# Kernel tuning notes

Hardware: AMD Instinct MI355X
Metric: run time of the kernel (lower is better)

## Reference

```python
import jax, jax.numpy as jnp
import numpy as np

B = 65536          # number of 17-node circle graphs in the batch
NN = 17            # nodes per graph (hardcoded in module)
FEAT = 32          # feature_num


def _circle_edge_index(num_graphs):
    s = np.arange(NN)
    d = (s + 1) % NN
    src0 = np.concatenate([s, d])   # bidirectional ring
    dst0 = np.concatenate([d, s])
    off = (np.arange(num_graphs) * NN)[:, None]
    src = (src0[None, :] + off).ravel()
    dst = (dst0[None, :] + off).ravel()
    return jnp.asarray(np.stack([src, dst]).astype(np.int32))


def setup_inputs() -> dict:
    key = jax.random.key(0)
    ks = jax.random.split(key, 10)
    p = lambda k, shp, fan: jax.random.normal(k, shp, jnp.float32) / np.sqrt(fan)
    return {
        "z": jax.random.normal(ks[0], (B, FEAT), jnp.float32),
        "edge_index": _circle_edge_index(B),                      # [2, 2*17*B]
        "fc_w": p(ks[1], (FEAT, NN * 8), FEAT),
        "fc_b": jnp.zeros((NN * 8,), jnp.float32),
        "w1": p(ks[2], (8, 16), 8),
        "b1": jnp.zeros((16,), jnp.float32),
        "w2": p(ks[3], (16, 32), 16),
        "b2": jnp.zeros((32,), jnp.float32),
        "w3": p(ks[4], (32, FEAT), 32),
        "b3": jnp.zeros((FEAT,), jnp.float32),
    }


def _gcn(x, src, tgt, norm, W, b, n_nodes):
    # GCNConv: out[t] = sum_{(s,t)} norm(s,t) * (x[s] @ W) + b
    h = x @ W
    msg = h[src] * norm[:, None]
    return jax.ops.segment_sum(msg, tgt, num_segments=n_nodes) + b


def reference(z, edge_index, fc_w, fc_b, w1, b1, w2, b2, w3, b3):
    n_nodes = z.shape[0] * NN
    # fc_expand then reshape to node features [N, 8]
    x = (z @ fc_w + fc_b).reshape(-1, 8)
    # symmetric GCN normalization with added self-loops (same for all 3 convs)
    loop = jnp.arange(n_nodes, dtype=edge_index.dtype)
    src = jnp.concatenate([edge_index[0], loop])
    tgt = jnp.concatenate([edge_index[1], loop])
    deg = jax.ops.segment_sum(jnp.ones_like(tgt, dtype=x.dtype), tgt,
                              num_segments=n_nodes)
    dinv = jax.lax.rsqrt(deg)  # deg >= 1 because of self-loops
    norm = dinv[src] * dinv[tgt]
    x = jax.nn.relu(_gcn(x, src, tgt, norm, w1, b1, n_nodes))
    x = jax.nn.relu(_gcn(x, src, tgt, norm, w2, b2, n_nodes))
    x = _gcn(x, src, tgt, norm, w3, b3, n_nodes)
    return x.reshape(-1, NN, FEAT)
```

## Files before the change

### kernel.cpp

```cpp
#include <hip/hip_runtime.h>
#include <stdint.h>

typedef unsigned short u16;
typedef unsigned int   u32;
typedef __attribute__((ext_vector_type(8))) short bf16x8;
typedef __attribute__((ext_vector_type(4))) float f32x4;

#define NN   17
#define G    16
#define ROWS (G*NN)
#define TPB  256
#define XS   40

__device__ u16   g_fcw_frag[9*512];
__device__ float g_fcb_agg[144];
__device__ u16   g_w1_frag[512];
__device__ u16   g_w2_frag[2*512];
__device__ u16   g_w3_frag[2*512];
__device__ float g_bias1[16];
__device__ float g_bias2[32];
__device__ float g_bias3[32];

__device__ __forceinline__ float uf(u32 u){ union{u32 a; float b;} c; c.a=u; return c.b; }
__device__ __forceinline__ u32   fu(float f){ union{float a; u32 b;} c; c.a=f; return c.b; }
__device__ __forceinline__ u16 f2bf(float f){
    u32 u = fu(f);
    return (u16)((u + 0x7FFFu + ((u >> 16) & 1u)) >> 16);
}
__device__ __forceinline__ bf16x8 as_bf16x8(uint4 v){ union{uint4 a; bf16x8 b;} c; c.a=v; return c.b; }

__device__ __forceinline__ u32 ringsum3(u32 a, u32 b, u32 c){
    const u32 M = 0xFFFF0000u;
    float hs = uf(a & M) + uf(b & M) + uf(c & M);
    float ls = uf(a << 16) + uf(b << 16) + uf(c << 16);
    u32 uh = fu(hs); uh = (uh + 0x7FFFu + ((uh >> 16) & 1u)) & M;
    u32 ul = fu(ls); ul = (ul + 0x7FFFu + ((ul >> 16) & 1u)) >> 16;
    return uh | ul;
}

__global__ void gnn_prep(const float* __restrict__ fcw, const float* __restrict__ fcb,
                         const float* __restrict__ w1,  const float* __restrict__ b1,
                         const float* __restrict__ w2,  const float* __restrict__ b2,
                         const float* __restrict__ w3,  const float* __restrict__ b3)
{
    const int t = threadIdx.x;
    const float inv3 = 1.0f/3.0f;
    for (int e = t; e < 9*512; e += TPB) {
        int tile = e >> 9, ln = (e >> 3) & 63, j = e & 7;
        int n = tile*16 + (ln & 15), k = (ln >> 4)*8 + j;
        u16 v = 0;
        if (n < 136) {
            int i = n >> 3, f = n & 7;
            int im = (i == 0    ? NN-1 : i-1)*8 + f;
            int ip = (i == NN-1 ? 0    : i+1)*8 + f;
            v = f2bf((fcw[k*136 + im] + fcw[k*136 + n] + fcw[k*136 + ip]) * inv3);
        }
        g_fcw_frag[e] = v;
    }
    if (t < 144) {
        float v = 0.f;
        if (t < 136) {
            int i = t >> 3, f = t & 7;
            int im = (i == 0    ? NN-1 : i-1)*8 + f;
            int ip = (i == NN-1 ? 0    : i+1)*8 + f;
            v = (fcb[im] + fcb[t] + fcb[ip]) * inv3;
        }
        g_fcb_agg[t] = v;
    }
    for (int e = t; e < 512; e += TPB) {
        int ln = e >> 3, j = e & 7;
        int k = (ln >> 4)*8 + j, n = ln & 15;
        g_w1_frag[e] = (k < 8) ? f2bf(w1[k*16 + n]) : (u16)0;
    }
    for (int e = t; e < 1024; e += TPB) {
        int h = e >> 9, ln = (e >> 3) & 63, j = e & 7;
        int k = ((ln >> 4))*8 + j, c = 2*(ln & 15) + h;
        g_w2_frag[e] = (k < 16) ? f2bf(w2[k*32 + c] * inv3) : (u16)0;
        g_w3_frag[e] = f2bf(w3[k*32 + c] * inv3);
    }
    if (t < 16)                 g_bias1[t]    = b1[t];
    else if (t >= 32 && t < 64) g_bias2[t-32] = b2[t-32];
    else if (t >= 64 && t < 96) g_bias3[t-64] = b3[t-64];
}

__global__ __launch_bounds__(TPB, 3)
void gnn_main(const float* __restrict__ z, float* __restrict__ out, int nG)
{
    __shared__ u16 xb0[ROWS*XS];
    __shared__ u16 xb1[ROWS*XS];
    __shared__ u16 zt [G*XS];

    const int t = threadIdx.x, wv = t >> 6, ln = t & 63;
    const int quad = ln >> 4, l16 = ln & 15;
    int gmax = nG - blockIdx.x * G; if (gmax > G) gmax = G;

    bf16x8 fw1  = *(const bf16x8*)(g_w1_frag + ln*8);
    bf16x8 fw2e = *(const bf16x8*)(g_w2_frag + ln*8);
    bf16x8 fw2o = *(const bf16x8*)(g_w2_frag + 512 + ln*8);
    bf16x8 fw3e = *(const bf16x8*)(g_w3_frag + ln*8);
    bf16x8 fw3o = *(const bf16x8*)(g_w3_frag + 512 + ln*8);
    bf16x8 ffc[3]; float fcbv[3];
    #pragma unroll
    for (int s = 0; s < 3; ++s) {
        int tile = wv + 4*s;
        if (tile < 9) {
            ffc[s]  = *(const bf16x8*)(g_fcw_frag + tile*512 + ln*8);
            fcbv[s] = g_fcb_agg[tile*16 + l16];
        } else { ffc[s] = (bf16x8){0,0,0,0,0,0,0,0}; fcbv[s] = 0.f; }
    }
    const float bias1 = g_bias1[l16];
    const float b2e = g_bias2[2*l16], b2o = g_bias2[2*l16+1];
    const float b3e = g_bias3[2*l16], b3o = g_bias3[2*l16+1];

    const float* zg = z + (size_t)blockIdx.x * (G*32);
    for (int el = t; el < G*32; el += TPB)
        if (el < gmax*32) zt[(el >> 5)*XS + (el & 31)] = f2bf(zg[el]);
    __syncthreads();

    {
        bf16x8 az = *(const bf16x8*)&zt[l16*XS + quad*8];
        #pragma unroll
        for (int s = 0; s < 3; ++s) {
            int tile = wv + 4*s;
            if (tile < 9) {
                f32x4 cb = {fcbv[s], fcbv[s], fcbv[s], fcbv[s]};
                f32x4 d = __builtin_amdgcn_mfma_f32_16x16x32_bf16(az, ffc[s], cb, 0, 0, 0);
                int n = tile*16 + l16;
                if (n < 136) {
                    int node = n >> 3, f = n & 7;
                    #pragma unroll
                    for (int r = 0; r < 4; ++r) {
                        int gg = quad*4 + r;
                        xb0[(gg*NN + node)*XS + f] = f2bf(d[r]);
                    }
                }
            }
        }
    }
    __syncthreads();

    {
        f32x4 cb = {bias1, bias1, bias1, bias1};
        #pragma unroll
        for (int s = 0; s < 5; ++s) {
            int tile = wv + 4*s;
            if (tile < 17) {
                bf16x8 af = {0,0,0,0,0,0,0,0};
                if (quad == 0) af = *(const bf16x8*)&xb0[(tile*16 + l16)*XS];
                f32x4 d = __builtin_amdgcn_mfma_f32_16x16x32_bf16(af, fw1, cb, 0, 0, 0);
                #pragma unroll
                for (int r = 0; r < 4; ++r) {
                    int rr = tile*16 + quad*4 + r;
                    xb1[rr*XS + l16] = f2bf(fmaxf(d[r], 0.f));
                }
            }
        }
    }
    __syncthreads();

    {
        f32x4 cbe = {b2e,b2e,b2e,b2e}, cbo = {b2o,b2o,b2o,b2o};
        #pragma unroll
        for (int s = 0; s < 5; ++s) {
            int tile = wv + 4*s;
            if (tile < 17) {
                bf16x8 af = {0,0,0,0,0,0,0,0};
                if (quad < 2) {
                    int rr = tile*16 + l16;
                    int gg = (rr*3856) >> 16; int i = rr - gg*NN;
                    int rm = rr + (i == 0    ? NN-1 : -1);
                    int rp = rr + (i == NN-1 ? 1-NN  :  1);
                    uint4 A  = *(const uint4*)&xb1[rm*XS + quad*8];
                    uint4 Bv = *(const uint4*)&xb1[rr*XS + quad*8];
                    uint4 Cv = *(const uint4*)&xb1[rp*XS + quad*8];
                    af = as_bf16x8(make_uint4(ringsum3(A.x,Bv.x,Cv.x), ringsum3(A.y,Bv.y,Cv.y),
                                              ringsum3(A.z,Bv.z,Cv.z), ringsum3(A.w,Bv.w,Cv.w)));
                }
                f32x4 d0 = __builtin_amdgcn_mfma_f32_16x16x32_bf16(af, fw2e, cbe, 0, 0, 0);
                f32x4 d1 = __builtin_amdgcn_mfma_f32_16x16x32_bf16(af, fw2o, cbo, 0, 0, 0);
                u32* ob = (u32*)xb0;
                #pragma unroll
                for (int r = 0; r < 4; ++r) {
                    int rr2 = tile*16 + quad*4 + r;
                    u32 ue = fu(fmaxf(d0[r], 0.f));
                    u32 uo = fu(fmaxf(d1[r], 0.f));
                    ue = (ue + 0x7FFFu + ((ue >> 16) & 1u)) >> 16;
                    uo = (uo + 0x7FFFu + ((uo >> 16) & 1u)) & 0xFFFF0000u;
                    ob[rr2*(XS/2) + l16] = ue | uo;
                }
            }
        }
    }
    __syncthreads();

    {
        f32x4 cbe = {b3e,b3e,b3e,b3e}, cbo = {b3o,b3o,b3o,b3o};
        float* ob = out + (size_t)blockIdx.x * (ROWS*32);
        const int rowmax = gmax * NN;
        #pragma unroll
        for (int s = 0; s < 5; ++s) {
            int tile = wv + 4*s;
            if (tile < 17) {
                int rr = tile*16 + l16;
                int gg = (rr*3856) >> 16; int i = rr - gg*NN;
                int rm = rr + (i == 0    ? NN-1 : -1);
                int rp = rr + (i == NN-1 ? 1-NN  :  1);
                uint4 A  = *(const uint4*)&xb0[rm*XS + quad*8];
                uint4 Bv = *(const uint4*)&xb0[rr*XS + quad*8];
                uint4 Cv = *(const uint4*)&xb0[rp*XS + quad*8];
                bf16x8 af = as_bf16x8(make_uint4(ringsum3(A.x,Bv.x,Cv.x), ringsum3(A.y,Bv.y,Cv.y),
                                                 ringsum3(A.z,Bv.z,Cv.z), ringsum3(A.w,Bv.w,Cv.w)));
                f32x4 d0 = __builtin_amdgcn_mfma_f32_16x16x32_bf16(af, fw3e, cbe, 0, 0, 0);
                f32x4 d1 = __builtin_amdgcn_mfma_f32_16x16x32_bf16(af, fw3o, cbo, 0, 0, 0);
                #pragma unroll
                for (int r = 0; r < 4; ++r) {
                    int rr2 = tile*16 + quad*4 + r;
                    if (rr2 < rowmax) {
                        float2 v = make_float2(d0[r], d1[r]);
                        *(float2*)&ob[(size_t)rr2*32 + 2*l16] = v;
                    }
                }
            }
        }
    }
}

extern "C" void kernel_launch(void* const* d_in, const int* in_sizes, int n_in,
                              void* d_out, int out_size, void* d_ws, size_t ws_size,
                              hipStream_t stream) {
    const float* z    = (const float*)d_in[0];
    const float* fcw  = (const float*)d_in[2];
    const float* fcb  = (const float*)d_in[3];
    const float* w1   = (const float*)d_in[4];
    const float* b1   = (const float*)d_in[5];
    const float* w2   = (const float*)d_in[6];
    const float* b2   = (const float*)d_in[7];
    const float* w3   = (const float*)d_in[8];
    const float* b3   = (const float*)d_in[9];
    float* out = (float*)d_out;

    const int nG   = in_sizes[0] / 32;
    const int grid = (nG + G - 1) / G;
    gnn_prep<<<1, TPB, 0, stream>>>(fcw, fcb, w1, b1, w2, b2, w3, b3);
    gnn_main<<<grid, TPB, 0, stream>>>(z, out, nG);
}
```

Measured before the change: 207.2 us.

## Fold fc_expand and first GCN layer into per-node precomputed weights

Precomputes, per node, the composition of the ring-averaged fc weights with w1 (and the matching bias), so the main kernel goes from z to layer-1 output with one MFMA per node tile. This removes the separate fc stage, one shared-memory round trip and one barrier. It also loads z straight into registers and narrows the layer-1 buffer stride to cut LDS use, raises the occupancy hint, and replaces manual bf16 rounding with the packed hardware convert instruction. The prep kernel now runs on multiple blocks. Folding the two matrices changes where bf16 rounding happens, which may shift numerics slightly.

```diff
diff --git a/kernel.cpp b/kernel.cpp
--- a/kernel.cpp
+++ b/kernel.cpp
@@ -10,14 +10,13 @@
 #define G    16
 #define ROWS (G*NN)
 #define TPB  256
-#define XS   40
-
-__device__ u16   g_fcw_frag[9*512];
-__device__ float g_fcb_agg[144];
-__device__ u16   g_w1_frag[512];
+#define XS1  24
+#define XS2  40
+
+__device__ u16   g_w1p_frag[NN*512];
+__device__ float g_b1p[ROWS];
 __device__ u16   g_w2_frag[2*512];
 __device__ u16   g_w3_frag[2*512];
-__device__ float g_bias1[16];
 __device__ float g_bias2[32];
 __device__ float g_bias3[32];
 
@@ -29,13 +28,15 @@
 }
 __device__ __forceinline__ bf16x8 as_bf16x8(uint4 v){ union{uint4 a; bf16x8 b;} c; c.a=v; return c.b; }
 
-__device__ __forceinline__ u32 ringsum3(u32 a, u32 b, u32 c){
+__device__ __forceinline__ u32 cvtpk(float lo, float hi){
+    u32 r; asm("v_cvt_pk_bf16_f32 %0, %1, %2" : "=v"(r) : "v"(lo), "v"(hi)); return r;
+}
+
+__device__ __forceinline__ u32 ringsum3_pk(u32 a, u32 b, u32 c){
     const u32 M = 0xFFFF0000u;
     float hs = uf(a & M) + uf(b & M) + uf(c & M);
     float ls = uf(a << 16) + uf(b << 16) + uf(c << 16);
-    u32 uh = fu(hs); uh = (uh + 0x7FFFu + ((uh >> 16) & 1u)) & M;
-    u32 ul = fu(ls); ul = (ul + 0x7FFFu + ((ul >> 16) & 1u)) >> 16;
-    return uh | ul;
+    return cvtpk(ls, hs);
 }
 
 __global__ void gnn_prep(const float* __restrict__ fcw, const float* __restrict__ fcb,
@@ -43,150 +44,125 @@
                          const float* __restrict__ w2,  const float* __restrict__ b2,
                          const float* __restrict__ w3,  const float* __restrict__ b3)
 {
-    const int t = threadIdx.x;
+    const int t = threadIdx.x, blk = blockIdx.x;
     const float inv3 = 1.0f/3.0f;
-    for (int e = t; e < 9*512; e += TPB) {
-        int tile = e >> 9, ln = (e >> 3) & 63, j = e & 7;
-        int n = tile*16 + (ln & 15), k = (ln >> 4)*8 + j;
-        u16 v = 0;
-        if (n < 136) {
-            int i = n >> 3, f = n & 7;
-            int im = (i == 0    ? NN-1 : i-1)*8 + f;
-            int ip = (i == NN-1 ? 0    : i+1)*8 + f;
-            v = f2bf((fcw[k*136 + im] + fcw[k*136 + n] + fcw[k*136 + ip]) * inv3);
-        }
-        g_fcw_frag[e] = v;
-    }
-    if (t < 144) {
-        float v = 0.f;
-        if (t < 136) {
-            int i = t >> 3, f = t & 7;
-            int im = (i == 0    ? NN-1 : i-1)*8 + f;
-            int ip = (i == NN-1 ? 0    : i+1)*8 + f;
-            v = (fcb[im] + fcb[t] + fcb[ip]) * inv3;
-        }
-        g_fcb_agg[t] = v;
-    }
-    for (int e = t; e < 512; e += TPB) {
-        int ln = e >> 3, j = e & 7;
-        int k = (ln >> 4)*8 + j, n = ln & 15;
-        g_w1_frag[e] = (k < 8) ? f2bf(w1[k*16 + n]) : (u16)0;
-    }
-    for (int e = t; e < 1024; e += TPB) {
-        int h = e >> 9, ln = (e >> 3) & 63, j = e & 7;
-        int k = ((ln >> 4))*8 + j, c = 2*(ln & 15) + h;
-        g_w2_frag[e] = (k < 16) ? f2bf(w2[k*32 + c] * inv3) : (u16)0;
-        g_w3_frag[e] = f2bf(w3[k*32 + c] * inv3);
-    }
-    if (t < 16)                 g_bias1[t]    = b1[t];
-    else if (t >= 32 && t < 64) g_bias2[t-32] = b2[t-32];
-    else if (t >= 64 && t < 96) g_bias3[t-64] = b3[t-64];
-}
-
-__global__ __launch_bounds__(TPB, 3)
+
+    if (blk < NN) {
+        __shared__ float s_avg[32][8];
+        __shared__ float s_w1[8][16];
+        const int i  = blk;
+        const int im = (i == 0    ? NN-1 : i-1);
+        const int ip = (i == NN-1 ? 0    : i+1);
+        {   int k = t >> 3, f = t & 7;
+            s_avg[k][f] = (fcw[k*136 + im*8+f] + fcw[k*136 + i*8+f] + fcw[k*136 + ip*8+f]) * inv3;
+        }
+        if (t < 128) s_w1[t >> 4][t & 15] = w1[t];
+        __syncthreads();
+        for (int e = t; e < 512; e += TPB) {
+            int ln = e >> 3, j = e & 7;
+            int k = (ln >> 4)*8 + j, c = ln & 15;
+            float v = 0.f;
+            #pragma unroll
+            for (int f = 0; f < 8; ++f) v += s_avg[k][f] * s_w1[f][c];
+            g_w1p_frag[i*512 + e] = f2bf(v);
+        }
+    } else {
+        for (int e = t; e < 1024; e += TPB) {
+            int h = e >> 9, ln = (e >> 3) & 63, j = e & 7;
+            int k = (ln >> 4)*8 + j, c = 2*(ln & 15) + h;
+            g_w2_frag[e] = (k < 16) ? f2bf(w2[k*32 + c] * inv3) : (u16)0;
+            g_w3_frag[e] = f2bf(w3[k*32 + c] * inv3);
+        }
+        if (t < 32) { g_bias2[t] = b2[t]; g_bias3[t] = b3[t]; }
+        for (int e = t; e < ROWS; e += TPB) {
+            int i = e >> 4, c = e & 15;
+            int im = (i == 0    ? NN-1 : i-1);
+            int ip = (i == NN-1 ? 0    : i+1);
+            float v = b1[c];
+            #pragma unroll
+            for (int f = 0; f < 8; ++f)
+                v += (fcb[im*8+f] + fcb[i*8+f] + fcb[ip*8+f]) * inv3 * w1[f*16 + c];
+            g_b1p[e] = v;
+        }
+    }
+}
+
+__global__ __launch_bounds__(TPB, 4)
 void gnn_main(const float* __restrict__ z, float* __restrict__ out, int nG)
 {
-    __shared__ u16 xb0[ROWS*XS];
-    __shared__ u16 xb1[ROWS*XS];
-    __shared__ u16 zt [G*XS];
+    __shared__ __align__(16) u16 x1[ROWS*XS1];
+    __shared__ __align__(16) u16 x2[ROWS*XS2];
 
     const int t = threadIdx.x, wv = t >> 6, ln = t & 63;
     const int quad = ln >> 4, l16 = ln & 15;
     int gmax = nG - blockIdx.x * G; if (gmax > G) gmax = G;
 
-    bf16x8 fw1  = *(const bf16x8*)(g_w1_frag + ln*8);
+    bf16x8 fw1t[5]; float b1v[5];
+    #pragma unroll
+    for (int s = 0; s < 5; ++s) {
+        int tile = wv + 4*s;
+        if (tile < NN) {
+            fw1t[s] = *(const bf16x8*)(g_w1p_frag + tile*512 + ln*8);
+            b1v[s]  = g_b1p[tile*16 + l16];
+        } else { fw1t[s] = (bf16x8){0,0,0,0,0,0,0,0}; b1v[s] = 0.f; }
+    }
     bf16x8 fw2e = *(const bf16x8*)(g_w2_frag + ln*8);
     bf16x8 fw2o = *(const bf16x8*)(g_w2_frag + 512 + ln*8);
     bf16x8 fw3e = *(const bf16x8*)(g_w3_frag + ln*8);
     bf16x8 fw3o = *(const bf16x8*)(g_w3_frag + 512 + ln*8);
-    bf16x8 ffc[3]; float fcbv[3];
-    #pragma unroll
-    for (int s = 0; s < 3; ++s) {
-        int tile = wv + 4*s;
-        if (tile < 9) {
-            ffc[s]  = *(const bf16x8*)(g_fcw_frag + tile*512 + ln*8);
-            fcbv[s] = g_fcb_agg[tile*16 + l16];
-        } else { ffc[s] = (bf16x8){0,0,0,0,0,0,0,0}; fcbv[s] = 0.f; }
-    }
-    const float bias1 = g_bias1[l16];
     const float b2e = g_bias2[2*l16], b2o = g_bias2[2*l16+1];
     const float b3e = g_bias3[2*l16], b3o = g_bias3[2*l16+1];
 
-    const float* zg = z + (size_t)blockIdx.x * (G*32);
-    for (int el = t; el < G*32; el += TPB)
-        if (el < gmax*32) zt[(el >> 5)*XS + (el & 31)] = f2bf(zg[el]);
+    bf16x8 az = (bf16x8){0,0,0,0,0,0,0,0};
+    if (l16 < gmax) {
+        const float* zp = z + ((size_t)blockIdx.x*G + l16)*32 + quad*8;
+        float4 a0 = *(const float4*)zp, a1 = *(const float4*)(zp + 4);
+        az = as_bf16x8(make_uint4(cvtpk(a0.x,a0.y), cvtpk(a0.z,a0.w),
+                                  cvtpk(a1.x,a1.y), cvtpk(a1.z,a1.w)));
+    }
+
+    #pragma unroll
+    for (int s = 0; s < 5; ++s) {
+        int tile = wv + 4*s;
+        if (tile < NN) {
+            f32x4 cb = {b1v[s], b1v[s], b1v[s], b1v[s]};
+            f32x4 d = __builtin_amdgcn_mfma_f32_16x16x32_bf16(az, fw1t[s], cb, 0, 0, 0);
+            u32 p01 = cvtpk(fmaxf(d[0],0.f), fmaxf(d[1],0.f));
+            u32 p23 = cvtpk(fmaxf(d[2],0.f), fmaxf(d[3],0.f));
+            int base = ((quad*4)*NN + tile)*XS1 + l16;
+            x1[base]              = (u16)p01;
+            x1[base +   NN*XS1]   = (u16)(p01 >> 16);
+            x1[base + 2*NN*XS1]   = (u16)p23;
+            x1[base + 3*NN*XS1]   = (u16)(p23 >> 16);
+        }
+    }
     __syncthreads();
 
     {
-        bf16x8 az = *(const bf16x8*)&zt[l16*XS + quad*8];
-        #pragma unroll
-        for (int s = 0; s < 3; ++s) {
-            int tile = wv + 4*s;
-            if (tile < 9) {
-                f32x4 cb = {fcbv[s], fcbv[s], fcbv[s], fcbv[s]};
-                f32x4 d = __builtin_amdgcn_mfma_f32_16x16x32_bf16(az, ffc[s], cb, 0, 0, 0);
-                int n = tile*16 + l16;
-                if (n < 136) {
-                    int node = n >> 3, f = n & 7;
-                    #pragma unroll
-                    for (int r = 0; r < 4; ++r) {
-                        int gg = quad*4 + r;
-                        xb0[(gg*NN + node)*XS + f] = f2bf(d[r]);
-                    }
-                }
-            }
-        }
-    }
-    __syncthreads();
-
-    {
-        f32x4 cb = {bias1, bias1, bias1, bias1};
+        f32x4 cbe = {b2e,b2e,b2e,b2e}, cbo = {b2o,b2o,b2o,b2o};
+        u32* ob2 = (u32*)x2;
         #pragma unroll
         for (int s = 0; s < 5; ++s) {
             int tile = wv + 4*s;
-            if (tile < 17) {
-                bf16x8 af = {0,0,0,0,0,0,0,0};
-                if (quad == 0) af = *(const bf16x8*)&xb0[(tile*16 + l16)*XS];
-                f32x4 d = __builtin_amdgcn_mfma_f32_16x16x32_bf16(af, fw1, cb, 0, 0, 0);
-                #pragma unroll
-                for (int r = 0; r < 4; ++r) {
-                    int rr = tile*16 + quad*4 + r;
-                    xb1[rr*XS + l16] = f2bf(fmaxf(d[r], 0.f));
-                }
-            }
-        }
-    }
-    __syncthreads();
-
-    {
-        f32x4 cbe = {b2e,b2e,b2e,b2e}, cbo = {b2o,b2o,b2o,b2o};
-        #pragma unroll
-        for (int s = 0; s < 5; ++s) {
-            int tile = wv + 4*s;
-            if (tile < 17) {
-                bf16x8 af = {0,0,0,0,0,0,0,0};
+            if (tile < NN) {
+                bf16x8 af = (bf16x8){0,0,0,0,0,0,0,0};
                 if (quad < 2) {
                     int rr = tile*16 + l16;
                     int gg = (rr*3856) >> 16; int i = rr - gg*NN;
                     int rm = rr + (i == 0    ? NN-1 : -1);
                     int rp = rr + (i == NN-1 ? 1-NN  :  1);
-                    uint4 A  = *(const uint4*)&xb1[rm*XS + quad*8];
-                    uint4 Bv = *(const uint4*)&xb1[rr*XS + quad*8];
-                    uint4 Cv = *(const uint4*)&xb1[rp*XS + quad*8];
-                    af = as_bf16x8(make_uint4(ringsum3(A.x,Bv.x,Cv.x), ringsum3(A.y,Bv.y,Cv.y),
-                                              ringsum3(A.z,Bv.z,Cv.z), ringsum3(A.w,Bv.w,Cv.w)));
+                    uint4 A  = *(const uint4*)&x1[rm*XS1 + quad*8];
+                    uint4 Bv = *(const uint4*)&x1[rr*XS1 + quad*8];
+                    uint4 Cv = *(const uint4*)&x1[rp*XS1 + quad*8];
+                    af = as_bf16x8(make_uint4(ringsum3_pk(A.x,Bv.x,Cv.x), ringsum3_pk(A.y,Bv.y,Cv.y),
+                                              ringsum3_pk(A.z,Bv.z,Cv.z), ringsum3_pk(A.w,Bv.w,Cv.w)));
                 }
                 f32x4 d0 = __builtin_amdgcn_mfma_f32_16x16x32_bf16(af, fw2e, cbe, 0, 0, 0);
                 f32x4 d1 = __builtin_amdgcn_mfma_f32_16x16x32_bf16(af, fw2o, cbo, 0, 0, 0);
-                u32* ob = (u32*)xb0;
                 #pragma unroll
                 for (int r = 0; r < 4; ++r) {
                     int rr2 = tile*16 + quad*4 + r;
-                    u32 ue = fu(fmaxf(d0[r], 0.f));
-                    u32 uo = fu(fmaxf(d1[r], 0.f));
-                    ue = (ue + 0x7FFFu + ((ue >> 16) & 1u)) >> 16;
-                    uo = (uo + 0x7FFFu + ((uo >> 16) & 1u)) & 0xFFFF0000u;
-                    ob[rr2*(XS/2) + l16] = ue | uo;
+                    ob2[rr2*(XS2/2) + l16] = cvtpk(fmaxf(d0[r],0.f), fmaxf(d1[r],0.f));
                 }
             }
         }
@@ -200,16 +176,16 @@
         #pragma unroll
         for (int s = 0; s < 5; ++s) {
             int tile = wv + 4*s;
-            if (tile < 17) {
+            if (tile < NN) {
                 int rr = tile*16 + l16;
                 int gg = (rr*3856) >> 16; int i = rr - gg*NN;
                 int rm = rr + (i == 0    ? NN-1 : -1);
                 int rp = rr + (i == NN-1 ? 1-NN  :  1);
-                uint4 A  = *(const uint4*)&xb0[rm*XS + quad*8];
-                uint4 Bv = *(const uint4*)&xb0[rr*XS + quad*8];
-                uint4 Cv = *(const uint4*)&xb0[rp*XS + quad*8];
-                bf16x8 af = as_bf16x8(make_uint4(ringsum3(A.x,Bv.x,Cv.x), ringsum3(A.y,Bv.y,Cv.y),
-                                                 ringsum3(A.z,Bv.z,Cv.z), ringsum3(A.w,Bv.w,Cv.w)));
+                uint4 A  = *(const uint4*)&x2[rm*XS2 + quad*8];
+                uint4 Bv = *(const uint4*)&x2[rr*XS2 + quad*8];
+                uint4 Cv = *(const uint4*)&x2[rp*XS2 + quad*8];
+                bf16x8 af = as_bf16x8(make_uint4(ringsum3_pk(A.x,Bv.x,Cv.x), ringsum3_pk(A.y,Bv.y,Cv.y),
+                                                 ringsum3_pk(A.z,Bv.z,Cv.z), ringsum3_pk(A.w,Bv.w,Cv.w)));
                 f32x4 d0 = __builtin_amdgcn_mfma_f32_16x16x32_bf16(af, fw3e, cbe, 0, 0, 0);
                 f32x4 d1 = __builtin_amdgcn_mfma_f32_16x16x32_bf16(af, fw3o, cbo, 0, 0, 0);
                 #pragma unroll
@@ -241,6 +217,6 @@
 
     const int nG   = in_sizes[0] / 32;
     const int grid = (nG + G - 1) / G;
-    gnn_prep<<<1, TPB, 0, stream>>>(fcw, fcb, w1, b1, w2, b2, w3, b3);
+    gnn_prep<<<NN + 1, TPB, 0, stream>>>(fcw, fcb, w1, b1, w2, b2, w3, b3);
     gnn_main<<<grid, TPB, 0, stream>>>(z, out, nG);
 }
```

New measurement: 187.2 us. -9.6%, faster.
